# Kernel tuning notes

Measured on AMD Instinct MI355X. Metric: run time of the kernel, lower is better.

The kernel has to match this reference:

```python
import jax, jax.numpy as jnp
import numpy as np

N_NODES = 50000
N_EDGES = 800000
IN_DIM = 128
HID_DIM = 128
OUT_DIM = 1


def _gcn_conv(x, edge_index, W, b):
    """PyG GCNConv: add self-loops, symmetric deg^{-1/2} normalization,
    x' = D^{-1/2}(A+I)D^{-1/2} (x @ W) + b."""
    n = x.shape[0]
    loop = jnp.arange(n, dtype=edge_index.dtype)
    src = jnp.concatenate([edge_index[0], loop])  # [E+N]
    dst = jnp.concatenate([edge_index[1], loop])  # [E+N]
    deg = jax.ops.segment_sum(jnp.ones(src.shape[0], dtype=x.dtype), dst,
                              num_segments=n)
    dinv = jnp.where(deg > 0, jax.lax.rsqrt(deg), jnp.zeros_like(deg))
    norm = dinv[src] * dinv[dst]                   # [E+N]
    h = x @ W                                      # [N, out]
    msg = h[src] * norm[:, None]                   # gather + scale
    out = jax.ops.segment_sum(msg, dst, num_segments=n)  # scatter-add
    return out + b


def setup_inputs() -> dict:
    key = jax.random.key(0)
    k0, k1, k2, k3 = jax.random.split(key, 4)
    x = jax.random.normal(k0, (N_NODES, IN_DIM), dtype=jnp.float32)
    edge_index = jax.random.randint(k1, (2, N_EDGES), 0, N_NODES, dtype=jnp.int64)
    W1 = jax.random.normal(k2, (IN_DIM, HID_DIM), dtype=jnp.float32) / np.sqrt(IN_DIM)
    b1 = jnp.zeros((HID_DIM,), dtype=jnp.float32)
    W2 = jax.random.normal(k3, (HID_DIM, OUT_DIM), dtype=jnp.float32) / np.sqrt(HID_DIM)
    b2 = jnp.zeros((OUT_DIM,), dtype=jnp.float32)
    return {"x": x, "edge_index": edge_index, "W1": W1, "b1": b1,
            "W2": W2, "b2": b2}


def reference(x, edge_index, W1, b1, W2, b2):
    h = _gcn_conv(x, edge_index, W1, b1)
    h = jax.nn.relu(h)
    out = _gcn_conv(h, edge_index, W2, b2)
    return out.squeeze(-1)  # [N]
```

## Files before the change

### kernel.cpp

```cpp
#include <hip/hip_runtime.h>
#include <hip/hip_fp16.h>

using f16x8 = __attribute__((ext_vector_type(8))) _Float16;
using f32x4 = __attribute__((ext_vector_type(4))) float;


__global__ void k_count_deg(const int* __restrict__ dst, int* __restrict__ deg, int e) {
    int i = blockIdx.x * blockDim.x + threadIdx.x;
    int stride = gridDim.x * blockDim.x;
    for (; i < e; i += stride) atomicAdd(&deg[dst[i]], 1);
}

__global__ __launch_bounds__(512) void k_scan1(const int* __restrict__ deg,
                                               float* __restrict__ dinv,
                                               int* __restrict__ bsum, int n) {
    int t = threadIdx.x;
    int i = blockIdx.x * 512 + t;
    int d = (i < n) ? deg[i] : 0;
    if (i < n) dinv[i] = rsqrtf((float)(d + 1));
    int v = d;
#pragma unroll
    for (int off = 32; off > 0; off >>= 1) v += __shfl_xor(v, off, 64);
    __shared__ int wsum[8];
    if ((t & 63) == 0) wsum[t >> 6] = v;
    __syncthreads();
    if (t == 0) {
        int s = 0;
#pragma unroll
        for (int j = 0; j < 8; ++j) s += wsum[j];
        bsum[blockIdx.x] = s;
    }
}

__global__ __launch_bounds__(512) void k_scan3(const int* __restrict__ deg,
                                               const int* __restrict__ bsum,
                                               int* __restrict__ rowptr, int n) {
    __shared__ int sm[512];
    __shared__ int sboff;
    int t = threadIdx.x;
    int v = (t < blockIdx.x) ? bsum[t] : 0;
#pragma unroll
    for (int off = 32; off > 0; off >>= 1) v += __shfl_xor(v, off, 64);
    if ((t & 63) == 0) sm[t >> 6] = v;
    __syncthreads();
    if (t == 0) {
        int s = 0;
#pragma unroll
        for (int j = 0; j < 8; ++j) s += sm[j];
        sboff = s;
    }
    __syncthreads();
    int boff = sboff;
    __syncthreads();
    int i = blockIdx.x * 512 + t;
    int d = (i < n) ? deg[i] : 0;
    sm[t] = d;
    __syncthreads();
    for (int dd = 1; dd < 512; dd <<= 1) {
        int vv = (t >= dd) ? sm[t - dd] : 0;
        __syncthreads();
        sm[t] += vv;
        __syncthreads();
    }
    int excl = sm[t] - d;
    if (i < n) {
        rowptr[i] = boff + excl;
        if (i == n - 1) rowptr[n] = boff + excl + d;
    }
}

__global__ void k_scatter(const int* __restrict__ src, const int* __restrict__ dst,
                          const int* __restrict__ rowptr, int* __restrict__ cursor,
                          const float* __restrict__ dinv,
                          int2* __restrict__ enorm, int e) {
    int i = blockIdx.x * blockDim.x + threadIdx.x;
    int stride = gridDim.x * blockDim.x;
    for (; i < e; i += stride) {
        int ss = src[i];
        int dd = dst[i];
        int pos = rowptr[dd] + atomicAdd(&cursor[dd], 1);
        float nn = dinv[ss] * dinv[dd];
        enorm[pos] = make_int2(ss, __float_as_int(nn));
    }
}


__global__ __launch_bounds__(256) void k_gemm1(const float* __restrict__ x,
                                               const float* __restrict__ W,
                                               __half* __restrict__ h1, int n) {
    __shared__ _Float16 Wf[8 * 4 * 64 * 8];
    int t = threadIdx.x;

    const float4* Wg4 = (const float4*)W;
#pragma unroll
    for (int ii = 0; ii < 16; ++ii) {
        int idx4 = t + 256 * ii;
        int k  = idx4 >> 5;
        int n0 = (idx4 & 31) * 4;
        float4 w = Wg4[idx4];
        int nt = n0 >> 4;
        int kc = k >> 5;
        int ln = ((k >> 3) & 3) * 16 + (n0 & 15);
        int i  = k & 7;
        int base = (((nt << 2) + kc) * 64 + ln) * 8 + i;
        Wf[base]      = (_Float16)w.x;
        Wf[base + 8]  = (_Float16)w.y;
        Wf[base + 16] = (_Float16)w.z;
        Wf[base + 24] = (_Float16)w.w;
    }
    __syncthreads();

    int lane = t & 63;
    int w_id = t >> 6;
    int row0 = blockIdx.x * 64 + w_id * 16;
    int arow = row0 + (lane & 15);
    if (arow >= n) arow = n - 1;
    int kb = (lane >> 4) * 8;

    f32x4 acc[8];
#pragma unroll
    for (int nt = 0; nt < 8; ++nt) acc[nt] = (f32x4){0.f, 0.f, 0.f, 0.f};

    const float* xr = x + (size_t)arow * 128;
#pragma unroll
    for (int kc = 0; kc < 4; ++kc) {
        float4 xa = *(const float4*)(xr + kc * 32 + kb);
        float4 xb = *(const float4*)(xr + kc * 32 + kb + 4);
        f16x8 a;
        a[0] = (_Float16)xa.x; a[1] = (_Float16)xa.y;
        a[2] = (_Float16)xa.z; a[3] = (_Float16)xa.w;
        a[4] = (_Float16)xb.x; a[5] = (_Float16)xb.y;
        a[6] = (_Float16)xb.z; a[7] = (_Float16)xb.w;
#pragma unroll
        for (int nt = 0; nt < 8; ++nt) {
            f16x8 b = *(const f16x8*)&Wf[(((nt << 2) + kc) * 64 + lane) * 8];
            acc[nt] = __builtin_amdgcn_mfma_f32_16x16x32_f16(a, b, acc[nt], 0, 0, 0);
        }
    }

    int drow = row0 + (lane >> 4) * 4;
#pragma unroll
    for (int r = 0; r < 4; ++r) {
        int grow = drow + r;
        if (grow < n) {
#pragma unroll
            for (int nt = 0; nt < 8; ++nt)
                h1[(size_t)grow * 128 + nt * 16 + (lane & 15)] =
                    __float2half(acc[nt][r]);
        }
    }
}


__global__ __launch_bounds__(256) void k_agg_s(
    const int* __restrict__ rowptr, const int2* __restrict__ enorm,
    const float* __restrict__ dinv, const __half* __restrict__ h1,
    const float* __restrict__ b1, const float* __restrict__ W2,
    float* __restrict__ s, int n) {
    int lane = threadIdx.x & 63;
    int wid = blockIdx.x * (blockDim.x >> 6) + (threadIdx.x >> 6);
    wid = __builtin_amdgcn_readfirstlane(wid);
    int nw = gridDim.x * (blockDim.x >> 6);
    float2 bb = ((const float2*)b1)[lane];
    float2 ww = ((const float2*)W2)[lane];
    for (int i = wid; i < n; i += nw) {
        float di = dinv[i];
        float2 acc = __half22float2(((const __half2*)(h1 + (size_t)i * 128))[lane]);
        float self = di * di;
        acc.x *= self; acc.y *= self;
        int j = rowptr[i], end = rowptr[i + 1];
        for (; j + 4 <= end; j += 4) {
            int2 e0 = enorm[j],     e1 = enorm[j + 1];
            int2 e2 = enorm[j + 2], e3 = enorm[j + 3];
            float n0 = __int_as_float(e0.y), n1 = __int_as_float(e1.y);
            float n2 = __int_as_float(e2.y), n3 = __int_as_float(e3.y);
            float2 v0 = __half22float2(((const __half2*)(h1 + (size_t)e0.x * 128))[lane]);
            float2 v1 = __half22float2(((const __half2*)(h1 + (size_t)e1.x * 128))[lane]);
            float2 v2 = __half22float2(((const __half2*)(h1 + (size_t)e2.x * 128))[lane]);
            float2 v3 = __half22float2(((const __half2*)(h1 + (size_t)e3.x * 128))[lane]);
            acc.x += v0.x * n0; acc.y += v0.y * n0;
            acc.x += v1.x * n1; acc.y += v1.y * n1;
            acc.x += v2.x * n2; acc.y += v2.y * n2;
            acc.x += v3.x * n3; acc.y += v3.y * n3;
        }
        for (; j < end; ++j) {
            int2 e0 = enorm[j];
            float nn = __int_as_float(e0.y);
            float2 v = __half22float2(((const __half2*)(h1 + (size_t)e0.x * 128))[lane]);
            acc.x += v.x * nn; acc.y += v.y * nn;
        }
        float p = fmaxf(acc.x + bb.x, 0.f) * ww.x + fmaxf(acc.y + bb.y, 0.f) * ww.y;
#pragma unroll
        for (int off = 32; off > 0; off >>= 1)
            p += __shfl_xor(p, off, 64);
        if (lane == 0) s[i] = p;
    }
}


__global__ void k_out2(const int* __restrict__ rowptr, const int2* __restrict__ enorm,
                       const float* __restrict__ dinv, const float* __restrict__ s,
                       const float* __restrict__ b2, float* __restrict__ out, int n) {
    int i = blockIdx.x * blockDim.x + threadIdx.x;
    if (i >= n) return;
    float di = dinv[i];
    float acc = di * di * s[i];
    int j = rowptr[i], end = rowptr[i + 1];
    for (; j < end; ++j) {
        int2 e0 = enorm[j];
        acc += __int_as_float(e0.y) * s[e0.x];
    }
    out[i] = b2[0] + acc;
}


extern "C" void kernel_launch(void* const* d_in, const int* in_sizes, int n_in,
                              void* d_out, int out_size, void* d_ws, size_t ws_size,
                              hipStream_t stream) {
    const float* x  = (const float*)d_in[0];
    const int*   ei = (const int*)d_in[1];
    const float* W1 = (const float*)d_in[2];
    const float* b1 = (const float*)d_in[3];
    const float* W2 = (const float*)d_in[4];
    const float* b2 = (const float*)d_in[5];
    float* out = (float*)d_out;

    int n = in_sizes[0] / 128;
    int e = in_sizes[1] / 2;
    const int* srcp = ei;
    const int* dstp = ei + e;

    char* ws = (char*)d_ws;
    size_t off = 0;
    auto take = [&](size_t bytes) -> char* {
        char* p = ws + off;
        off += (bytes + 255) & ~(size_t)255;
        return p;
    };
    int*    deg    = (int*)take((size_t)n * 4);
    int*    cursor = (int*)take((size_t)n * 4);
    int*    rowptr = (int*)take((size_t)(n + 1) * 4);
    float*  dinv   = (float*)take((size_t)n * 4);
    float*  s      = (float*)take((size_t)n * 4);
    int2*   enorm  = (int2*)take((size_t)e * 8);
    int*    bsum   = (int*)take((size_t)512 * 4);
    __half* h1     = (__half*)take((size_t)n * 128 * 2);
    (void)ws_size;

    int egrid = (e + 255) / 256; if (egrid > 2048) egrid = 2048;
    int ngrid = (n + 255) / 256;
    int nscan = (n + 511) / 512;

    hipMemsetAsync(deg, 0, (((size_t)n * 4 + 255) & ~(size_t)255) + (size_t)n * 4, stream);

    hipLaunchKernelGGL(k_count_deg, dim3(egrid), dim3(256), 0, stream, dstp, deg, e);
    hipLaunchKernelGGL(k_scan1, dim3(nscan), dim3(512), 0, stream, deg, dinv, bsum, n);
    hipLaunchKernelGGL(k_scan3, dim3(nscan), dim3(512), 0, stream, deg, bsum, rowptr, n);
    hipLaunchKernelGGL(k_scatter, dim3(egrid), dim3(256), 0, stream,
                       srcp, dstp, rowptr, cursor, dinv, enorm, e);
    hipLaunchKernelGGL(k_gemm1, dim3((n + 63) / 64), dim3(256), 0, stream,
                       x, W1, h1, n);
    hipLaunchKernelGGL(k_agg_s, dim3(2048), dim3(256), 0, stream,
                       rowptr, enorm, dinv, h1, b1, W2, s, n);
    hipLaunchKernelGGL(k_out2, dim3(ngrid), dim3(256), 0, stream,
                       rowptr, enorm, dinv, s, b2, out, n);
}
```

Before: 218.8 us.

## Record edge slot during degree count; deepen gather unrolling in aggregation kernels

The degree-count kernel now stores the return value of its atomicAdd as each edge's slot within its destination row. The fill kernel then places edges using rowptr plus that slot, which removes the second round of 800k atomics and the cursor buffer and its memset. The layer-1 aggregation now issues 8 edge loads and 8 feature-row gathers before accumulating, up from 4, and the layer-2 scalar aggregation gains a 4-way unroll with separate accumulators to expose more memory-level parallelism. The cost is an extra 4-byte-per-edge pos array that must be written and read back, plus more registers in the aggregation kernel.

```diff
diff --git a/kernel.cpp b/kernel.cpp
--- a/kernel.cpp
+++ b/kernel.cpp
@@ -5,10 +5,11 @@
 using f32x4 = __attribute__((ext_vector_type(4))) float;
 
 
-__global__ void k_count_deg(const int* __restrict__ dst, int* __restrict__ deg, int e) {
+__global__ void k_count_pos(const int* __restrict__ dst, int* __restrict__ deg,
+                            int* __restrict__ pos, int e) {
     int i = blockIdx.x * blockDim.x + threadIdx.x;
     int stride = gridDim.x * blockDim.x;
-    for (; i < e; i += stride) atomicAdd(&deg[dst[i]], 1);
+    for (; i < e; i += stride) pos[i] = atomicAdd(&deg[dst[i]], 1);
 }
 
 __global__ __launch_bounds__(512) void k_scan1(const int* __restrict__ deg,
@@ -69,18 +70,17 @@
     }
 }
 
-__global__ void k_scatter(const int* __restrict__ src, const int* __restrict__ dst,
-                          const int* __restrict__ rowptr, int* __restrict__ cursor,
-                          const float* __restrict__ dinv,
-                          int2* __restrict__ enorm, int e) {
+__global__ void k_fill(const int* __restrict__ src, const int* __restrict__ dst,
+                       const int* __restrict__ pos, const int* __restrict__ rowptr,
+                       const float* __restrict__ dinv,
+                       int2* __restrict__ enorm, int e) {
     int i = blockIdx.x * blockDim.x + threadIdx.x;
     int stride = gridDim.x * blockDim.x;
     for (; i < e; i += stride) {
         int ss = src[i];
         int dd = dst[i];
-        int pos = rowptr[dd] + atomicAdd(&cursor[dd], 1);
         float nn = dinv[ss] * dinv[dd];
-        enorm[pos] = make_int2(ss, __float_as_int(nn));
+        enorm[rowptr[dd] + pos[i]] = make_int2(ss, __float_as_int(nn));
     }
 }
 
@@ -169,19 +169,20 @@
         float self = di * di;
         acc.x *= self; acc.y *= self;
         int j = rowptr[i], end = rowptr[i + 1];
-        for (; j + 4 <= end; j += 4) {
-            int2 e0 = enorm[j],     e1 = enorm[j + 1];
-            int2 e2 = enorm[j + 2], e3 = enorm[j + 3];
-            float n0 = __int_as_float(e0.y), n1 = __int_as_float(e1.y);
-            float n2 = __int_as_float(e2.y), n3 = __int_as_float(e3.y);
-            float2 v0 = __half22float2(((const __half2*)(h1 + (size_t)e0.x * 128))[lane]);
-            float2 v1 = __half22float2(((const __half2*)(h1 + (size_t)e1.x * 128))[lane]);
-            float2 v2 = __half22float2(((const __half2*)(h1 + (size_t)e2.x * 128))[lane]);
-            float2 v3 = __half22float2(((const __half2*)(h1 + (size_t)e3.x * 128))[lane]);
-            acc.x += v0.x * n0; acc.y += v0.y * n0;
-            acc.x += v1.x * n1; acc.y += v1.y * n1;
-            acc.x += v2.x * n2; acc.y += v2.y * n2;
-            acc.x += v3.x * n3; acc.y += v3.y * n3;
+        for (; j + 8 <= end; j += 8) {
+            int2 er[8];
+#pragma unroll
+            for (int q = 0; q < 8; ++q) er[q] = enorm[j + q];
+            __half2 vh[8];
+#pragma unroll
+            for (int q = 0; q < 8; ++q)
+                vh[q] = ((const __half2*)(h1 + (size_t)er[q].x * 128))[lane];
+#pragma unroll
+            for (int q = 0; q < 8; ++q) {
+                float nn = __int_as_float(er[q].y);
+                float2 v = __half22float2(vh[q]);
+                acc.x += v.x * nn; acc.y += v.y * nn;
+            }
         }
         for (; j < end; ++j) {
             int2 e0 = enorm[j];
@@ -206,6 +207,17 @@
     float di = dinv[i];
     float acc = di * di * s[i];
     int j = rowptr[i], end = rowptr[i + 1];
+    float a0 = 0.f, a1 = 0.f, a2 = 0.f, a3 = 0.f;
+    for (; j + 4 <= end; j += 4) {
+        int2 e0 = enorm[j],     e1 = enorm[j + 1];
+        int2 e2 = enorm[j + 2], e3 = enorm[j + 3];
+        float s0 = s[e0.x], s1 = s[e1.x], s2 = s[e2.x], s3 = s[e3.x];
+        a0 += __int_as_float(e0.y) * s0;
+        a1 += __int_as_float(e1.y) * s1;
+        a2 += __int_as_float(e2.y) * s2;
+        a3 += __int_as_float(e3.y) * s3;
+    }
+    acc += (a0 + a1) + (a2 + a3);
     for (; j < end; ++j) {
         int2 e0 = enorm[j];
         acc += __int_as_float(e0.y) * s[e0.x];
@@ -238,10 +250,10 @@
         return p;
     };
     int*    deg    = (int*)take((size_t)n * 4);
-    int*    cursor = (int*)take((size_t)n * 4);
     int*    rowptr = (int*)take((size_t)(n + 1) * 4);
     float*  dinv   = (float*)take((size_t)n * 4);
     float*  s      = (float*)take((size_t)n * 4);
+    int*    pos    = (int*)take((size_t)e * 4);
     int2*   enorm  = (int2*)take((size_t)e * 8);
     int*    bsum   = (int*)take((size_t)512 * 4);
     __half* h1     = (__half*)take((size_t)n * 128 * 2);
@@ -251,13 +263,14 @@
     int ngrid = (n + 255) / 256;
     int nscan = (n + 511) / 512;
 
-    hipMemsetAsync(deg, 0, (((size_t)n * 4 + 255) & ~(size_t)255) + (size_t)n * 4, stream);
-
-    hipLaunchKernelGGL(k_count_deg, dim3(egrid), dim3(256), 0, stream, dstp, deg, e);
+    hipMemsetAsync(deg, 0, (size_t)n * 4, stream);
+
+    hipLaunchKernelGGL(k_count_pos, dim3(egrid), dim3(256), 0, stream,
+                       dstp, deg, pos, e);
     hipLaunchKernelGGL(k_scan1, dim3(nscan), dim3(512), 0, stream, deg, dinv, bsum, n);
     hipLaunchKernelGGL(k_scan3, dim3(nscan), dim3(512), 0, stream, deg, bsum, rowptr, n);
-    hipLaunchKernelGGL(k_scatter, dim3(egrid), dim3(256), 0, stream,
-                       srcp, dstp, rowptr, cursor, dinv, enorm, e);
+    hipLaunchKernelGGL(k_fill, dim3(egrid), dim3(256), 0, stream,
+                       srcp, dstp, pos, rowptr, dinv, enorm, e);
     hipLaunchKernelGGL(k_gemm1, dim3((n + 63) / 64), dim3(256), 0, stream,
                        x, W1, h1, n);
     hipLaunchKernelGGL(k_agg_s, dim3(2048), dim3(256), 0, stream,
```

Result: faster. 190.7 us (-12.9%).
